# Performance work log

Measured on AMD Instinct MI355X. Metric: run time of the kernel, lower is better.

The kernel has to match this reference:

```python
import jax, jax.numpy as jnp
import numpy as np

K = 3  # spline order
G = 5  # grid_size

def bspline(x):
    # Cox-de Boor B-spline basis over uniform grid on [-1,1] extended by K knots each side.
    h = 2.0 / G
    grid = jnp.arange(-K, G + K + 1, dtype=x.dtype) * h - 1.0  # [G+2K+1]
    xe = x[..., None]
    b = ((xe >= grid[:-1]) & (xe < grid[1:])).astype(x.dtype)  # order-0 bases [..., G+2K]
    for p in range(1, K + 1):
        b = ((xe - grid[:-(p + 1)]) / (grid[p:-1] - grid[:-(p + 1)]) * b[..., :-1]
             + (grid[p + 1:] - xe) / (grid[p + 1:] - grid[1:-p]) * b[..., 1:])
    return b  # [..., G+K]

def kan_conv(x, wb, ws, k):
    # x: [B,Cin,H,W] -> patches [B, Cin*k*k, H', W'] -> KANLinear per spatial position
    p = jax.lax.conv_general_dilated_patches(x, (k, k), (1, 1), 'VALID')
    p = jnp.moveaxis(p, 1, -1)  # [B,H',W',F]
    base = jax.nn.silu(p) @ wb.T
    spline = jnp.einsum('bhwig,oig->bhwo', bspline(p), ws)
    return jnp.moveaxis(base + spline, -1, 1)  # [B,Cout,H',W']

def maxpool2(x):
    return jax.lax.reduce_window(x, -jnp.inf, jax.lax.max, (1, 1, 2, 2), (1, 1, 2, 2), 'VALID')

def setup_inputs() -> dict:
    key = jax.random.key(0)
    ks = jax.random.split(key, 9)
    B = 4096
    s = 0.1
    return {
        'x': jax.random.normal(ks[0], (B, 1, 28, 28), jnp.float32),
        'wb1': jax.random.normal(ks[1], (5, 9), jnp.float32) * s,
        'ws1': jax.random.normal(ks[2], (5, 9, G + K), jnp.float32) * s,
        'wb2': jax.random.normal(ks[3], (5, 125), jnp.float32) * s,
        'ws2': jax.random.normal(ks[4], (5, 125, G + K), jnp.float32) * s,
        'wb3': jax.random.normal(ks[5], (2, 45), jnp.float32) * s,
        'ws3': jax.random.normal(ks[6], (2, 45, G + K), jnp.float32) * s,
        'fc_w': jax.random.normal(ks[7], (200, 98), jnp.float32) * s,
        'fc_b': jnp.zeros((200,), jnp.float32),
    }

def reference(x, wb1, ws1, wb2, ws2, wb3, ws3, fc_w, fc_b):
    h = kan_conv(x, wb1, ws1, 3)    # [B,5,26,26]
    h = maxpool2(h)                 # [B,5,13,13]
    h = kan_conv(h, wb2, ws2, 5)    # [B,5,9,9]
    h = kan_conv(h, wb3, ws3, 3)    # [B,2,7,7]
    h = h.reshape(h.shape[0], -1)   # [B,98]
    return h @ fc_w.T + fc_b        # [B,200]
```

## Files before the change

### kernel.cpp

```cpp
#include <hip/hip_runtime.h>


typedef _Float16 h2 __attribute__((ext_vector_type(2)));
typedef _Float16 f16x8 __attribute__((ext_vector_type(8)));
typedef float f32x4 __attribute__((ext_vector_type(4)));
typedef unsigned int uint_t;
typedef unsigned long long u64;

__device__ __forceinline__ h2 as_h2(uint_t u) { union { uint_t u; h2 h; } c; c.u = u; return c.h; }
__device__ __forceinline__ uint_t pk(float a, float b) {
    h2 v; v[0] = (_Float16)a; v[1] = (_Float16)b;
    union { h2 h; uint_t u; } c; c.h = v; return c.u;
}

__device__ __forceinline__ float fdot2f(h2 a, h2 b, float c) {
#if __has_builtin(__builtin_amdgcn_fdot2)
    return __builtin_amdgcn_fdot2(a, b, c, false);
#else
    return c + (float)a[0] * (float)b[0] + (float)a[1] * (float)b[1];
#endif
}

__device__ __forceinline__ float silu_f(float v) {
    return v / (1.0f + __expf(-v));
}

struct RecW { u64 R0, R1; uint_t R2; };
__device__ __forceinline__ RecW rec_words(float v) {
    float s  = silu_f(v);
    float t  = (v + 2.2f) * 2.5f;
    float cf = floorf(t);
    int   c  = (int)cf;
    float u  = t - cf;
    float u2 = u * u, u3 = u2 * u;
    float w  = 1.0f - u;
    const float k6 = 0.16666667f;
    float n0 = k6 * u3;
    float n1 = k6 * (-3.0f * u3 + 3.0f * u2 + 3.0f * u + 1.0f);
    float n2 = k6 * (3.0f * u3 - 6.0f * u2 + 4.0f);
    float n3 = k6 * (w * w * w);
    u64 H = ((u64)pk(n1, n0) << 32) | (u64)pk(n3, n2);
    if ((unsigned)c > 10u) H = 0;
    int cc = c < 0 ? 0 : (c > 10 ? 10 : c);
    int L  = cc * 16 - 48;
    u64 sl_lo = (L < 64) ? (H << (L & 63)) : 0;
    u64 hi_a  = (L == 0) ? 0 : (H >> ((64 - L) & 63));
    u64 hi_b  = H << ((L - 64) & 63);
    u64 sl_hi = (L < 64) ? hi_a : hi_b;
    u64 sr    = H >> ((-L) & 63);
    u64 B0 = (L >= 0) ? sl_lo : sr;
    u64 B1 = (L >= 0) ? sl_hi : 0;
    RecW r;
    r.R0 = (B0 << 16) | (u64)pk(s, 0.0f);
    r.R1 = (B0 >> 48) | (B1 << 16);
    r.R2 = (uint_t)(B1 >> 48);
    return r;
}

__device__ __forceinline__ void write_rec16s(_Float16* p, int off, float v) {
    RecW rw = rec_words(v);
    uint4 lo, hi;
    lo.x = (uint_t)rw.R0; lo.y = (uint_t)(rw.R0 >> 32);
    lo.z = (uint_t)rw.R1; lo.w = (uint_t)(rw.R1 >> 32);
    hi.x = rw.R2; hi.y = 0; hi.z = 0; hi.w = 0;
    *(uint4*)(p + off)       = lo;
    *(uint4*)(p + (8 ^ off)) = hi;
}

__device__ __forceinline__ void write_rec10(_Float16* p, float v) {
    RecW rw = rec_words(v);
    uint_t* d = (uint_t*)p;
    d[0] = (uint_t)rw.R0; d[1] = (uint_t)(rw.R0 >> 32);
    d[2] = (uint_t)rw.R1; d[3] = (uint_t)(rw.R1 >> 32);
    d[4] = rw.R2;
}

struct Rec { h2 a[5]; };
__device__ __forceinline__ Rec load_rec16(const _Float16* p) {
    uint4  u0 = *(const uint4*)(p);
    uint_t u2 = *(const uint_t*)(p + 8);
    Rec r;
    r.a[0] = as_h2(u0.x); r.a[1] = as_h2(u0.y);
    r.a[2] = as_h2(u0.z); r.a[3] = as_h2(u0.w);
    r.a[4] = as_h2(u2);
    return r;
}

#define W3_OFF 6700
#define FCWT_BYTE_OFF  15360
#define W1COL_BYTE_OFF 93760
#define W2COL_BYTE_OFF 95680

__global__ __launch_bounds__(256) void kan_prep(
    const float* __restrict__ wb1, const float* __restrict__ ws1,
    const float* __restrict__ wb2, const float* __restrict__ ws2,
    const float* __restrict__ wb3, const float* __restrict__ ws3,
    const float* __restrict__ fcw, _Float16* __restrict__ w16,
    float* __restrict__ fcwT)
{
    _Float16* w1col = (_Float16*)((char*)w16 + W1COL_BYTE_OFF);
    _Float16* w2col = (_Float16*)((char*)w16 + W2COL_BYTE_OFF);
    int gtid = blockIdx.x * 256 + threadIdx.x;
    int gstr = gridDim.x * 256;
    for (int i = gtid; i < 760; i += gstr) {
        const float *wb, *ws; int r;
        if (i < 45)       { wb = wb1; ws = ws1; r = i; }
        else if (i < 670) { wb = wb2; ws = ws2; r = i - 45; }
        else              { wb = wb3; ws = ws3; r = i - 670; }
        _Float16* p = w16 + i * 10;
        p[0] = (_Float16)wb[r];
#pragma unroll
        for (int g = 0; g < 8; ++g) p[1 + g] = (_Float16)ws[r * 8 + g];
        p[9] = (_Float16)0.0f;
    }
    for (int i = gtid; i < 19600; i += gstr) {
        int o = i / 98, j = i % 98;
        fcwT[j * 200 + o] = fcw[i];
    }
    for (int i = gtid; i < 960; i += gstr) {
        int n = i / 160, k = i % 160;
        int rec = k >> 4, f = k & 15;
        float v = 0.f;
        if (n < 5 && rec < 9 && f < 10)
            v = (f == 0) ? wb1[n * 9 + rec] : ws1[(n * 9 + rec) * 8 + (f - 1)];
        w1col[i] = (_Float16)v;
    }
    for (int i = gtid; i < 9600; i += gstr) {
        int n = i / 1600, k2 = i % 1600;
        int tap = k2 >> 6, k = k2 & 63;
        int di = tap / 5, dj = tap % 5;
        int c = k / 10, f = k % 10;
        float v = 0.f;
        if (n < 5 && k < 50 && f < 9) {
            int r = n * 125 + c * 25 + di * 5 + dj;
            v = (f == 0) ? wb2[r] : ws2[r * 8 + (f - 1)];
        }
        w2col[i] = (_Float16)v;
    }
}

__global__ __launch_bounds__(256) void kan_fused(
    const float* __restrict__ x,
    const _Float16* __restrict__ w16,
    const _Float16* __restrict__ w1col,
    const _Float16* __restrict__ w2col,
    const float* __restrict__ fcwT,
    const float* __restrict__ fcb,
    float* __restrict__ out)
{
    __shared__ __align__(16) _Float16 smemA[12544];
    __shared__ __align__(16) float    smemB[1696];
    _Float16* P2h   = (_Float16*)smemB;
    float*    part2 = smemB;
    float*    part3 = smemB;
    float*    h3f   = smemB + 512;

    const int b   = blockIdx.x;
    const int tid = threadIdx.x;
    const int wv  = __builtin_amdgcn_readfirstlane(tid >> 6);
    const int ln  = tid & 63;

    const int m   = ln & 15;
    const int kb  = ln >> 4;
    const int hr  = kb >> 1;
    const int s8  = (kb & 1) * 8;
    const int nn  = m < 5 ? m : 5;

#pragma unroll 1
    for (int i = tid; i < 784; i += 256)
        write_rec16s(&smemA[i * 16], (i & 4) << 1, x[b * 784 + i]);
    __syncthreads();

    {
        f16x8 Bf[5];
#pragma unroll
        for (int ks = 0; ks < 5; ++ks)
            Bf[ks] = *(const f16x8*)(w1col + nn * 160 + ks * 32 + kb * 8);
        const int dpix[10] = {0, 1, 2, 28, 29, 30, 56, 57, 58, 0};
#pragma unroll 1
        for (int tile = wv; tile < 43; tile += 4) {
            int p = tile * 16 + m; p = p > 675 ? 675 : p;
            int pix0 = (p / 26) * 28 + (p % 26);
            f32x4 acc = {0.f, 0.f, 0.f, 0.f};
#pragma unroll
            for (int ks = 0; ks < 5; ++ks) {
                int dp = hr ? dpix[2 * ks + 1] : dpix[2 * ks];
                int p2 = pix0 + dp;
                int addr = p2 * 16 + (s8 ^ ((p2 & 4) << 1));
                f16x8 av = *(const f16x8*)(smemA + addr);
                acc = __builtin_amdgcn_mfma_f32_16x16x32_f16(av, Bf[ks], acc, 0, 0, 0);
            }
            int srow = tile * 16 + (ln >> 4) * 4;
#pragma unroll
            for (int r = 0; r < 4; ++r) {
                int s = srow + r;
                if (m < 5 && s < 676) P2h[m * 676 + s] = (_Float16)acc[r];
            }
        }
    }
    __syncthreads();

#pragma unroll 1
    for (int i = tid; i < 845; i += 256) {
        int c = i / 169, pp = i % 169;
        int ph = pp / 13, pw = pp % 13;
        const _Float16* q = P2h + c * 676 + (2 * ph) * 26 + 2 * pw;
        h2 a = as_h2(*(const uint_t*)q);
        h2 d = as_h2(*(const uint_t*)(q + 26));
        float mx = fmaxf(fmaxf((float)a[0], (float)a[1]),
                         fmaxf((float)d[0], (float)d[1]));
        write_rec10(&smemA[pp * 72 + c * 10], mx);
    }
    __syncthreads();

    {
        int ryb[6];
#pragma unroll
        for (int t = 0; t < 6; ++t) {
            int p = t * 16 + m; p = p > 80 ? 80 : p;
            ryb[t] = (p / 9) * 13 + (p % 9);
        }
        f32x4 acc[6];
#pragma unroll
        for (int t = 0; t < 6; ++t) { f32x4 z = {0.f,0.f,0.f,0.f}; acc[t] = z; }
#pragma unroll 1
        for (int tap = wv; tap < 25; tap += 4) {
            int di = tap / 5, dj = tap % 5;
            const _Float16* wrow = w2col + nn * 1600 + tap * 64 + kb * 8;
            f16x8 bv0 = *(const f16x8*)(wrow);
            f16x8 bv1 = *(const f16x8*)(wrow + 32);
            int qoff = di * 13 + dj;
#pragma unroll
            for (int t = 0; t < 6; ++t) {
                const _Float16* ab = smemA + (ryb[t] + qoff) * 72 + kb * 8;
                acc[t] = __builtin_amdgcn_mfma_f32_16x16x32_f16(
                             *(const f16x8*)(ab), bv0, acc[t], 0, 0, 0);
                acc[t] = __builtin_amdgcn_mfma_f32_16x16x32_f16(
                             *(const f16x8*)(ab + 32), bv1, acc[t], 0, 0, 0);
            }
        }
        int prow = (ln >> 4) * 4;
#pragma unroll
        for (int t = 0; t < 6; ++t) {
#pragma unroll
            for (int r = 0; r < 4; ++r) {
                int pp = t * 16 + prow + r;
                if (m < 5 && pp < 81) part2[(wv * 5 + m) * 81 + pp] = acc[t][r];
            }
        }
    }
    __syncthreads();

#pragma unroll 1
    for (int i = tid; i < 405; i += 256) {
        int o = i / 81, pp = i % 81;
        float v = part2[(0 * 5 + o) * 81 + pp] + part2[(1 * 5 + o) * 81 + pp]
                + part2[(2 * 5 + o) * 81 + pp] + part2[(3 * 5 + o) * 81 + pp];
        write_rec16s(&smemA[pp * 80 + o * 16], 0, v);
    }
    __syncthreads();

#pragma unroll 1
    for (int c = wv; c < 5; c += 4) {
        if (ln < 49) {
            int pp = ln;
            int y = pp / 7, xx = pp % 7;
            float acc[2] = {0.f, 0.f};
#pragma unroll 1
            for (int di = 0; di < 3; ++di) {
                const _Float16* base = &smemA[((y + di) * 9 + xx) * 80 + c * 16];
                Rec r[3];
#pragma unroll
                for (int p = 0; p < 3; ++p) r[p] = load_rec16(base + p * 80);
#pragma unroll
                for (int o = 0; o < 2; ++o) {
                    const h2* w = (const h2*)(w16 + (W3_OFF + (o * 45 + c * 9 + di * 3) * 10));
                    float a = acc[o];
#pragma unroll
                    for (int dj = 0; dj < 3; ++dj)
#pragma unroll
                        for (int q = 0; q < 5; ++q)
                            a = fdot2f(r[dj].a[q], w[dj * 5 + q], a);
                    acc[o] = a;
                }
            }
            part3[(c * 2 + 0) * 49 + pp] = acc[0];
            part3[(c * 2 + 1) * 49 + pp] = acc[1];
        }
    }
    __syncthreads();

    if (tid < 98) {
        int o = tid / 49, pp = tid % 49;
        float v = part3[(0 * 2 + o) * 49 + pp] + part3[(1 * 2 + o) * 49 + pp]
                + part3[(2 * 2 + o) * 49 + pp] + part3[(3 * 2 + o) * 49 + pp]
                + part3[(4 * 2 + o) * 49 + pp];
        h3f[tid] = v;
    }
    __syncthreads();

    if (tid < 200) {
        float a0 = 0.f, a1 = 0.f;
#pragma unroll 7
        for (int j = 0; j < 98; j += 2) {
            a0 += fcwT[j * 200 + tid]       * h3f[j];
            a1 += fcwT[(j + 1) * 200 + tid] * h3f[j + 1];
        }
        out[b * 200 + tid] = fcb[tid] + a0 + a1;
    }
}

extern "C" void kernel_launch(void* const* d_in, const int* in_sizes, int n_in,
                              void* d_out, int out_size, void* d_ws, size_t ws_size,
                              hipStream_t stream) {
    const float* x   = (const float*)d_in[0];
    const float* wb1 = (const float*)d_in[1];
    const float* ws1 = (const float*)d_in[2];
    const float* wb2 = (const float*)d_in[3];
    const float* ws2 = (const float*)d_in[4];
    const float* wb3 = (const float*)d_in[5];
    const float* ws3 = (const float*)d_in[6];
    const float* fcw = (const float*)d_in[7];
    const float* fcb = (const float*)d_in[8];
    float* out = (float*)d_out;

    _Float16* w16   = (_Float16*)d_ws;
    float*    fcwT  = (float*)((char*)d_ws + FCWT_BYTE_OFF);
    _Float16* w1col = (_Float16*)((char*)d_ws + W1COL_BYTE_OFF);
    _Float16* w2col = (_Float16*)((char*)d_ws + W2COL_BYTE_OFF);

    kan_prep<<<32, 256, 0, stream>>>(wb1, ws1, wb2, ws2, wb3, ws3, fcw, w16, fcwT);

    int B = in_sizes[0] / 784;
    kan_fused<<<B, 256, 0, stream>>>(x, w16, w1col, w2col, fcwT, fcb, out);
}
```

Measured before the change: 148.4 us.

## Move layer-3 KAN conv to MFMA and restructure layer-2 split and pooling

Layer 3 now runs as an MFMA implicit GEMM with a prepacked w3col weight layout, replacing the per-thread fdot2 loop and its cross-warp partial reduction. Layer 2 partitions output tiles across warps instead of taps, so the four-way partial-sum reduction goes away. Layer-1 outputs are written into unused slots of the input record buffer and max-pooled straight from there into registers, which shrinks shared memory. The aim is less LDS traffic, fewer reductions and higher occupancy, at the cost of uneven warp work in layer 2 and padded MFMA work in layer 3.

```diff
diff --git a/kernel.cpp b/kernel.cpp
--- a/kernel.cpp
+++ b/kernel.cpp
@@ -7,18 +7,9 @@
 typedef unsigned int uint_t;
 typedef unsigned long long u64;
 
-__device__ __forceinline__ h2 as_h2(uint_t u) { union { uint_t u; h2 h; } c; c.u = u; return c.h; }
 __device__ __forceinline__ uint_t pk(float a, float b) {
     h2 v; v[0] = (_Float16)a; v[1] = (_Float16)b;
     union { h2 h; uint_t u; } c; c.h = v; return c.u;
-}
-
-__device__ __forceinline__ float fdot2f(h2 a, h2 b, float c) {
-#if __has_builtin(__builtin_amdgcn_fdot2)
-    return __builtin_amdgcn_fdot2(a, b, c, false);
-#else
-    return c + (float)a[0] * (float)b[0] + (float)a[1] * (float)b[1];
-#endif
 }
 
 __device__ __forceinline__ float silu_f(float v) {
@@ -75,44 +66,21 @@
     d[4] = rw.R2;
 }
 
-struct Rec { h2 a[5]; };
-__device__ __forceinline__ Rec load_rec16(const _Float16* p) {
-    uint4  u0 = *(const uint4*)(p);
-    uint_t u2 = *(const uint_t*)(p + 8);
-    Rec r;
-    r.a[0] = as_h2(u0.x); r.a[1] = as_h2(u0.y);
-    r.a[2] = as_h2(u0.z); r.a[3] = as_h2(u0.w);
-    r.a[4] = as_h2(u2);
-    return r;
-}
-
-#define W3_OFF 6700
-#define FCWT_BYTE_OFF  15360
-#define W1COL_BYTE_OFF 93760
-#define W2COL_BYTE_OFF 95680
+#define FCWT_BYTE_OFF   0
+#define W1COL_BYTE_OFF  78400
+#define W2COL_BYTE_OFF  80320
+#define W3COL_BYTE_OFF  99520
 
 __global__ __launch_bounds__(256) void kan_prep(
     const float* __restrict__ wb1, const float* __restrict__ ws1,
     const float* __restrict__ wb2, const float* __restrict__ ws2,
     const float* __restrict__ wb3, const float* __restrict__ ws3,
-    const float* __restrict__ fcw, _Float16* __restrict__ w16,
-    float* __restrict__ fcwT)
+    const float* __restrict__ fcw, float* __restrict__ fcwT,
+    _Float16* __restrict__ w1col, _Float16* __restrict__ w2col,
+    _Float16* __restrict__ w3col)
 {
-    _Float16* w1col = (_Float16*)((char*)w16 + W1COL_BYTE_OFF);
-    _Float16* w2col = (_Float16*)((char*)w16 + W2COL_BYTE_OFF);
     int gtid = blockIdx.x * 256 + threadIdx.x;
     int gstr = gridDim.x * 256;
-    for (int i = gtid; i < 760; i += gstr) {
-        const float *wb, *ws; int r;
-        if (i < 45)       { wb = wb1; ws = ws1; r = i; }
-        else if (i < 670) { wb = wb2; ws = ws2; r = i - 45; }
-        else              { wb = wb3; ws = ws3; r = i - 670; }
-        _Float16* p = w16 + i * 10;
-        p[0] = (_Float16)wb[r];
-#pragma unroll
-        for (int g = 0; g < 8; ++g) p[1 + g] = (_Float16)ws[r * 8 + g];
-        p[9] = (_Float16)0.0f;
-    }
     for (int i = gtid; i < 19600; i += gstr) {
         int o = i / 98, j = i % 98;
         fcwT[j * 200 + o] = fcw[i];
@@ -121,7 +89,7 @@
         int n = i / 160, k = i % 160;
         int rec = k >> 4, f = k & 15;
         float v = 0.f;
-        if (n < 5 && rec < 9 && f < 10)
+        if (n < 5 && rec < 9 && f < 9)
             v = (f == 0) ? wb1[n * 9 + rec] : ws1[(n * 9 + rec) * 8 + (f - 1)];
         w1col[i] = (_Float16)v;
     }
@@ -137,23 +105,33 @@
         }
         w2col[i] = (_Float16)v;
     }
+    for (int i = gtid; i < 3456; i += gstr) {
+        int n = i / 576, k2 = i % 576;
+        int tap = k2 >> 6, k = k2 & 63;
+        int di = tap / 3, dj = tap % 3;
+        int c = k / 10, f = k % 10;
+        float v = 0.f;
+        if (n < 2 && k < 50 && f < 9) {
+            int r = n * 45 + c * 9 + di * 3 + dj;
+            v = (f == 0) ? wb3[r] : ws3[r * 8 + (f - 1)];
+        }
+        w3col[i] = (_Float16)v;
+    }
 }
 
 __global__ __launch_bounds__(256) void kan_fused(
     const float* __restrict__ x,
-    const _Float16* __restrict__ w16,
     const _Float16* __restrict__ w1col,
     const _Float16* __restrict__ w2col,
+    const _Float16* __restrict__ w3col,
     const float* __restrict__ fcwT,
     const float* __restrict__ fcb,
     float* __restrict__ out)
 {
     __shared__ __align__(16) _Float16 smemA[12544];
-    __shared__ __align__(16) float    smemB[1696];
-    _Float16* P2h   = (_Float16*)smemB;
-    float*    part2 = smemB;
-    float*    part3 = smemB;
-    float*    h3f   = smemB + 512;
+    __shared__ __align__(16) float    smemB[504];
+    float* buf = smemB;
+    float* h3f = smemB + 405;
 
     const int b   = blockIdx.x;
     const int tid = threadIdx.x;
@@ -190,112 +168,109 @@
                 f16x8 av = *(const f16x8*)(smemA + addr);
                 acc = __builtin_amdgcn_mfma_f32_16x16x32_f16(av, Bf[ks], acc, 0, 0, 0);
             }
-            int srow = tile * 16 + (ln >> 4) * 4;
+            int srow = tile * 16 + kb * 4;
 #pragma unroll
             for (int r = 0; r < 4; ++r) {
                 int s = srow + r;
-                if (m < 5 && s < 676) P2h[m * 676 + s] = (_Float16)acc[r];
+                if (m < 5 && s < 676)
+                    smemA[s * 16 + (8 ^ ((s & 4) << 1)) + 2 + m] = (_Float16)acc[r];
             }
         }
     }
     __syncthreads();
 
-#pragma unroll 1
-    for (int i = tid; i < 845; i += 256) {
-        int c = i / 169, pp = i % 169;
-        int ph = pp / 13, pw = pp % 13;
-        const _Float16* q = P2h + c * 676 + (2 * ph) * 26 + 2 * pw;
-        h2 a = as_h2(*(const uint_t*)q);
-        h2 d = as_h2(*(const uint_t*)(q + 26));
-        float mx = fmaxf(fmaxf((float)a[0], (float)a[1]),
-                         fmaxf((float)d[0], (float)d[1]));
-        write_rec10(&smemA[pp * 72 + c * 10], mx);
-    }
-    __syncthreads();
-
-    {
-        int ryb[6];
-#pragma unroll
-        for (int t = 0; t < 6; ++t) {
-            int p = t * 16 + m; p = p > 80 ? 80 : p;
-            ryb[t] = (p / 9) * 13 + (p % 9);
-        }
-        f32x4 acc[6];
-#pragma unroll
-        for (int t = 0; t < 6; ++t) { f32x4 z = {0.f,0.f,0.f,0.f}; acc[t] = z; }
-#pragma unroll 1
-        for (int tap = wv; tap < 25; tap += 4) {
+    float mx0, mx1, mx2, mx3 = 0.f;
+    {
+        auto pool = [&](int i) -> float {
+            int pp = i / 5, c = i % 5;
+            int ph = pp / 13, pw = pp % 13;
+            int s0 = ph * 52 + pw * 2;
+            int s1 = s0 + 1, s2 = s0 + 26, s3 = s0 + 27;
+            float v00 = (float)smemA[s0 * 16 + (8 ^ ((s0 & 4) << 1)) + 2 + c];
+            float v01 = (float)smemA[s1 * 16 + (8 ^ ((s1 & 4) << 1)) + 2 + c];
+            float v10 = (float)smemA[s2 * 16 + (8 ^ ((s2 & 4) << 1)) + 2 + c];
+            float v11 = (float)smemA[s3 * 16 + (8 ^ ((s3 & 4) << 1)) + 2 + c];
+            return fmaxf(fmaxf(v00, v01), fmaxf(v10, v11));
+        };
+        mx0 = pool(tid);
+        mx1 = pool(tid + 256);
+        mx2 = pool(tid + 512);
+        if (tid < 77) mx3 = pool(tid + 768);
+    }
+    __syncthreads();
+
+    {
+        auto st = [&](int i, float v) {
+            int pp = i / 5, c = i % 5;
+            write_rec10(&smemA[pp * 72 + c * 10], v);
+        };
+        st(tid, mx0);
+        st(tid + 256, mx1);
+        st(tid + 512, mx2);
+        if (tid < 77) st(tid + 768, mx3);
+    }
+    __syncthreads();
+
+    {
+        int p0 = wv * 16 + m;       p0 = p0 > 80 ? 80 : p0;
+        int p1 = (wv + 4) * 16 + m; p1 = p1 > 80 ? 80 : p1;
+        int ry0 = (p0 / 9) * 13 + (p0 % 9);
+        int ry1 = (p1 / 9) * 13 + (p1 % 9);
+        const bool two = (wv < 2);
+        f32x4 acc0 = {0.f, 0.f, 0.f, 0.f}, acc1 = {0.f, 0.f, 0.f, 0.f};
+#pragma unroll 1
+        for (int tap = 0; tap < 25; ++tap) {
             int di = tap / 5, dj = tap % 5;
             const _Float16* wrow = w2col + nn * 1600 + tap * 64 + kb * 8;
             f16x8 bv0 = *(const f16x8*)(wrow);
             f16x8 bv1 = *(const f16x8*)(wrow + 32);
             int qoff = di * 13 + dj;
-#pragma unroll
-            for (int t = 0; t < 6; ++t) {
-                const _Float16* ab = smemA + (ryb[t] + qoff) * 72 + kb * 8;
-                acc[t] = __builtin_amdgcn_mfma_f32_16x16x32_f16(
-                             *(const f16x8*)(ab), bv0, acc[t], 0, 0, 0);
-                acc[t] = __builtin_amdgcn_mfma_f32_16x16x32_f16(
-                             *(const f16x8*)(ab + 32), bv1, acc[t], 0, 0, 0);
+            const _Float16* ab0 = smemA + (ry0 + qoff) * 72 + kb * 8;
+            acc0 = __builtin_amdgcn_mfma_f32_16x16x32_f16(*(const f16x8*)(ab0),      bv0, acc0, 0, 0, 0);
+            acc0 = __builtin_amdgcn_mfma_f32_16x16x32_f16(*(const f16x8*)(ab0 + 32), bv1, acc0, 0, 0, 0);
+            if (two) {
+                const _Float16* ab1 = smemA + (ry1 + qoff) * 72 + kb * 8;
+                acc1 = __builtin_amdgcn_mfma_f32_16x16x32_f16(*(const f16x8*)(ab1),      bv0, acc1, 0, 0, 0);
+                acc1 = __builtin_amdgcn_mfma_f32_16x16x32_f16(*(const f16x8*)(ab1 + 32), bv1, acc1, 0, 0, 0);
             }
         }
-        int prow = (ln >> 4) * 4;
-#pragma unroll
-        for (int t = 0; t < 6; ++t) {
-#pragma unroll
-            for (int r = 0; r < 4; ++r) {
-                int pp = t * 16 + prow + r;
-                if (m < 5 && pp < 81) part2[(wv * 5 + m) * 81 + pp] = acc[t][r];
-            }
+        int prow = kb * 4;
+#pragma unroll
+        for (int r = 0; r < 4; ++r) {
+            int pp0 = wv * 16 + prow + r;
+            if (m < 5 && pp0 < 81) buf[m * 81 + pp0] = acc0[r];
+            int pp1 = (wv + 4) * 16 + prow + r;
+            if (two && m < 5 && pp1 < 81) buf[m * 81 + pp1] = acc1[r];
         }
     }
     __syncthreads();
 
 #pragma unroll 1
     for (int i = tid; i < 405; i += 256) {
-        int o = i / 81, pp = i % 81;
-        float v = part2[(0 * 5 + o) * 81 + pp] + part2[(1 * 5 + o) * 81 + pp]
-                + part2[(2 * 5 + o) * 81 + pp] + part2[(3 * 5 + o) * 81 + pp];
-        write_rec16s(&smemA[pp * 80 + o * 16], 0, v);
-    }
-    __syncthreads();
-
-#pragma unroll 1
-    for (int c = wv; c < 5; c += 4) {
-        if (ln < 49) {
-            int pp = ln;
-            int y = pp / 7, xx = pp % 7;
-            float acc[2] = {0.f, 0.f};
-#pragma unroll 1
-            for (int di = 0; di < 3; ++di) {
-                const _Float16* base = &smemA[((y + di) * 9 + xx) * 80 + c * 16];
-                Rec r[3];
-#pragma unroll
-                for (int p = 0; p < 3; ++p) r[p] = load_rec16(base + p * 80);
-#pragma unroll
-                for (int o = 0; o < 2; ++o) {
-                    const h2* w = (const h2*)(w16 + (W3_OFF + (o * 45 + c * 9 + di * 3) * 10));
-                    float a = acc[o];
-#pragma unroll
-                    for (int dj = 0; dj < 3; ++dj)
-#pragma unroll
-                        for (int q = 0; q < 5; ++q)
-                            a = fdot2f(r[dj].a[q], w[dj * 5 + q], a);
-                    acc[o] = a;
-                }
-            }
-            part3[(c * 2 + 0) * 49 + pp] = acc[0];
-            part3[(c * 2 + 1) * 49 + pp] = acc[1];
-        }
-    }
-    __syncthreads();
-
-    if (tid < 98) {
-        int o = tid / 49, pp = tid % 49;
-        float v = part3[(0 * 2 + o) * 49 + pp] + part3[(1 * 2 + o) * 49 + pp]
-                + part3[(2 * 2 + o) * 49 + pp] + part3[(3 * 2 + o) * 49 + pp]
-                + part3[(4 * 2 + o) * 49 + pp];
-        h3f[tid] = v;
+        int pp = i / 5, o = i % 5;
+        write_rec10(&smemA[pp * 72 + o * 10], buf[o * 81 + pp]);
+    }
+    __syncthreads();
+
+    {
+        int p3 = wv * 16 + m; p3 = p3 > 48 ? 48 : p3;
+        int ry3 = (p3 / 7) * 9 + (p3 % 7);
+        f32x4 acc = {0.f, 0.f, 0.f, 0.f};
+#pragma unroll 1
+        for (int tap = 0; tap < 9; ++tap) {
+            int di = tap / 3, dj = tap % 3;
+            const _Float16* wrow = w3col + nn * 576 + tap * 64 + kb * 8;
+            f16x8 bv0 = *(const f16x8*)(wrow);
+            f16x8 bv1 = *(const f16x8*)(wrow + 32);
+            const _Float16* ab = smemA + (ry3 + di * 9 + dj) * 72 + kb * 8;
+            acc = __builtin_amdgcn_mfma_f32_16x16x32_f16(*(const f16x8*)(ab),      bv0, acc, 0, 0, 0);
+            acc = __builtin_amdgcn_mfma_f32_16x16x32_f16(*(const f16x8*)(ab + 32), bv1, acc, 0, 0, 0);
+        }
+#pragma unroll
+        for (int r = 0; r < 4; ++r) {
+            int pout = wv * 16 + kb * 4 + r;
+            if (m < 2 && pout < 49) h3f[m * 49 + pout] = acc[r];
+        }
     }
     __syncthreads();
 
@@ -324,13 +299,14 @@
     const float* fcb = (const float*)d_in[8];
     float* out = (float*)d_out;
 
-    _Float16* w16   = (_Float16*)d_ws;
     float*    fcwT  = (float*)((char*)d_ws + FCWT_BYTE_OFF);
     _Float16* w1col = (_Float16*)((char*)d_ws + W1COL_BYTE_OFF);
     _Float16* w2col = (_Float16*)((char*)d_ws + W2COL_BYTE_OFF);
-
-    kan_prep<<<32, 256, 0, stream>>>(wb1, ws1, wb2, ws2, wb3, ws3, fcw, w16, fcwT);
+    _Float16* w3col = (_Float16*)((char*)d_ws + W3COL_BYTE_OFF);
+
+    kan_prep<<<32, 256, 0, stream>>>(wb1, ws1, wb2, ws2, wb3, ws3, fcw,
+                                     fcwT, w1col, w2col, w3col);
 
     int B = in_sizes[0] / 784;
-    kan_fused<<<B, 256, 0, stream>>>(x, w16, w1col, w2col, fcwT, fcb, out);
-}
+    kan_fused<<<B, 256, 0, stream>>>(x, w1col, w2col, w3col, fcwT, fcb, out);
+}
```

Result: slower. 169.8 us (+14.4%).
